# Optimization experiments

Hardware: AMD Instinct MI355X
Metric: run time of the kernel (lower is better)

The kernel has to match this reference:

```python
import jax, jax.numpy as jnp
import numpy as np

WIDTH = 256          # hidden width of FiLM MLP
NUM_FREQ = 8         # NeRF frequencies
BASE_FREQ = 1.25
TWO_PI = 2.0 * np.pi


def _uniform_linear(k, out_dim, in_dim):
    # torch nn.Linear default init: U(-1/sqrt(in), 1/sqrt(in))
    kw, kb = jax.random.split(k)
    s = 1.0 / np.sqrt(in_dim)
    W = jax.random.uniform(kw, (out_dim, in_dim), minval=-s, maxval=s, dtype=jnp.float32)
    b = jax.random.uniform(kb, (out_dim,), minval=-s, maxval=s, dtype=jnp.float32)
    return W, b


def setup_inputs() -> dict:
    key = jax.random.key(0)
    ks = jax.random.split(key, 14)
    B, T = 1024, 512
    latent_dim, lstm_hidden_dim = 128, 128
    spatial_dim, dir_dim, num_directions = 32, 8, 6
    emb_out = 2 * NUM_FREQ + 1                      # 17 (include_input)
    mod_in = latent_dim + lstm_hidden_dim + spatial_dim + dir_dim  # 296
    num_mods = 2 * WIDTH                            # width*(depth-1) = 512

    W_mod, b_mod = _uniform_linear(ks[0], num_mods, mod_in)
    W0, b0 = _uniform_linear(ks[1], WIDTH, emb_out)
    W1, b1 = _uniform_linear(ks[2], WIDTH, WIDTH)
    Wo, bo = _uniform_linear(ks[3], 1, WIDTH)
    Bmat = jax.random.normal(ks[4], (2, 16), dtype=jnp.float32) * 0.1  # sigma=0.1
    Ws1, bs1 = _uniform_linear(ks[5], 64, 32)
    Ws2, bs2 = _uniform_linear(ks[6], spatial_dim, 64)
    dir_emb = jax.random.normal(ks[7], (num_directions, dir_dim), dtype=jnp.float32)

    return dict(
        coords=jax.random.uniform(ks[8], (B, T, 1), dtype=jnp.float32),
        code=jax.random.normal(ks[9], (B, latent_dim), dtype=jnp.float32),
        hs=jax.random.normal(ks[10], (B, T, lstm_hidden_dim), dtype=jnp.float32),
        x_statics=jax.random.normal(ks[11], (B, 2), dtype=jnp.float32),
        dir_idx=jax.random.randint(ks[12], (1024,), 0, num_directions, dtype=jnp.int32),
        W_mod=W_mod, b_mod=b_mod, W0=W0, b0=b0, W1=W1, b1=b1, Wo=Wo, bo=bo,
        Bmat=Bmat, Ws1=Ws1, bs1=bs1, Ws2=Ws2, bs2=bs2, dir_emb=dir_emb,
    )


def reference(coords, code, hs, x_statics, dir_idx,
              W_mod, b_mod, W0, b0, W1, b1, Wo, bo,
              Bmat, Ws1, bs1, Ws2, bs2, dir_emb):
    B, T, _ = coords.shape

    # --- NeRF encoding: (B,T,1) -> (B,T,17) ---
    bands = BASE_FREQ * jnp.arange(0, NUM_FREQ, dtype=coords.dtype)     # (8,)
    winded = (coords[..., None, :] * bands[None, None, :, None]).reshape(B, T, -1)
    pos = jnp.concatenate([coords, jnp.sin(winded), jnp.cos(winded)], axis=-1)

    # --- Static encoder: latlon Fourier MLP + direction embedding ---
    proj = TWO_PI * (x_statics @ Bmat)                                  # (B,16)
    feats = jnp.concatenate([jnp.sin(proj), jnp.cos(proj)], axis=-1)    # (B,32)
    h = jax.nn.gelu(feats @ Ws1.T + bs1, approximate=False)             # (B,64)
    spatial = h @ Ws2.T + bs2                                           # (B,32)
    static_emb = jnp.concatenate([spatial, dir_emb[dir_idx]], axis=-1)  # (B,40)

    # --- Modulations: cat(code, h_t, static) -> 2*WIDTH, vectorized over T ---
    ctx = jnp.concatenate([
        jnp.broadcast_to(code[:, None, :], (B, T, code.shape[-1])),
        hs,
        jnp.broadcast_to(static_emb[:, None, :], (B, T, static_emb.shape[-1])),
    ], axis=-1)                                                         # (B,T,296)
    mods = jnp.einsum('btc,mc->btm', ctx, W_mod) + b_mod                # (B,T,512)

    # --- FiLM(shift)-modulated MLP: relu(Lin(x) + mod_chunk) per hidden layer ---
    x = jax.nn.relu(jnp.einsum('bte,we->btw', pos, W0) + b0 + mods[..., :WIDTH])
    x = jax.nn.relu(jnp.einsum('btw,vw->btv', x, W1) + b1 + mods[..., WIDTH:])
    out = jnp.einsum('btw,ow->bto', x, Wo) + bo                         # (B,T,1)
    return out
```

## Files before the change

kernel.cpp:

```cpp
#include <hip/hip_runtime.h>
#include <math.h>

typedef unsigned short ushort_t;
typedef __bf16 bf16x8 __attribute__((ext_vector_type(8)));
typedef __bf16 bf16x4 __attribute__((ext_vector_type(4)));
typedef float f32x4 __attribute__((ext_vector_type(4)));

#define TWO_PI_F 6.283185307179586f

#define WMT_OFF   0
#define PC_OFF    151552
#define WT0P_OFF  675840
#define WT1P_OFF  696320

__device__ __forceinline__ ushort_t f2bf(float f) {
  unsigned int u = __float_as_uint(f);
  u += 0x7fffu + ((u >> 16) & 1u);
  return (ushort_t)(u >> 16);
}

__global__ void pack_mfma_k(const float* __restrict__ W0,
                            const float* __restrict__ W1,
                            const float* __restrict__ W_mod,
                            float* __restrict__ WmT,
                            ushort_t* __restrict__ WT0p,
                            ushort_t* __restrict__ WT1p) {
  int i0 = blockIdx.x * blockDim.x + threadIdx.x;
  int stride = gridDim.x * blockDim.x;
  for (int idx = i0; idx < 296 * 512; idx += stride) {
    int c = idx >> 9, m = idx & 511;
    WmT[idx] = W_mod[m * 296 + c];
  }
  for (int e = i0; e < 40960; e += stride) {
    int j = e & 7, l = (e >> 3) & 63, nt = (e >> 9) & 15, ks = e >> 13;
    int k = ks * 32 + (l >> 4) * 8 + j;
    int n = nt * 16 + (l & 15);
    float v = 0.0f;
    if (k < 17) v = W0[n * 17 + k];
    else if (k >= 32) v = W_mod[n * 296 + 128 + (k - 32)];
    WT0p[e] = f2bf(v);
  }
  for (int e = i0; e < 98304; e += stride) {
    int j = e & 7, l = (e >> 3) & 63, nt = (e >> 9) & 15, ks = e >> 13;
    int k = ks * 32 + (l >> 4) * 8 + j;
    int n = nt * 16 + (l & 15);
    float v = (k < 256) ? W1[n * 256 + k]
                        : W_mod[(256 + n) * 296 + 128 + (k - 256)];
    WT1p[e] = f2bf(v);
  }
}

__global__ void precompute_pc_k(const float* __restrict__ code,
                                const float* __restrict__ x_statics,
                                const int* __restrict__ dir_idx,
                                const float* __restrict__ WmT,
                                const float* __restrict__ b_mod,
                                const float* __restrict__ b0,
                                const float* __restrict__ b1,
                                const float* __restrict__ Bmat,
                                const float* __restrict__ Ws1,
                                const float* __restrict__ bs1,
                                const float* __restrict__ Ws2,
                                const float* __restrict__ bs2,
                                const float* __restrict__ dir_emb,
                                float* __restrict__ pc) {
  int b = blockIdx.x, t = threadIdx.x;
  __shared__ float feats[32];
  __shared__ float h[64];
  __shared__ float se[40];
  __shared__ float cd[128];
  if (t < 16) {
    float p = TWO_PI_F * (x_statics[2 * b] * Bmat[t] + x_statics[2 * b + 1] * Bmat[16 + t]);
    feats[t] = sinf(p);
    feats[16 + t] = cosf(p);
  }
  if (t >= 128 && t < 256) cd[t - 128] = code[b * 128 + (t - 128)];
  __syncthreads();
  if (t < 64) {
    float a = bs1[t];
#pragma unroll
    for (int c = 0; c < 32; ++c) a = fmaf(feats[c], Ws1[t * 32 + c], a);
    h[t] = 0.5f * a * (1.0f + erff(a * 0.70710678118654752440f));
  }
  __syncthreads();
  if (t < 32) {
    float a = bs2[t];
#pragma unroll
    for (int c = 0; c < 64; ++c) a = fmaf(h[c], Ws2[t * 64 + c], a);
    se[t] = a;
  } else if (t < 40) {
    se[t] = dir_emb[dir_idx[b] * 8 + (t - 32)];
  }
  __syncthreads();
  float a = b_mod[t] + ((t < 256) ? b0[t] : b1[t - 256]);
  for (int c = 0; c < 128; ++c) a = fmaf(cd[c], WmT[c * 512 + t], a);
#pragma unroll
  for (int c = 0; c < 40; ++c) a = fmaf(se[c], WmT[(256 + c) * 512 + t], a);
  pc[b * 512 + t] = a;
}

__global__ __launch_bounds__(512, 6) void film_mfma(
    const float* __restrict__ coords, const float* __restrict__ hs,
    const float* __restrict__ pc, const ushort_t* __restrict__ WT0p,
    const ushort_t* __restrict__ WT1p, const float* __restrict__ Wo,
    const float* __restrict__ bo, float* __restrict__ out) {
  __shared__ uint4 rowbuf4[49152 / 16];
  __shared__ float pcs[512];
  __shared__ float psum[512];
  char* rowbuf = (char*)rowbuf4;

  const int tid = threadIdx.x;
  const int wv = tid >> 6;
  const int l = tid & 63;
  const int l4 = l & 15;
  const int hi4 = l >> 4;
  const size_t row0 = (size_t)blockIdx.x * 64;
  const int b = blockIdx.x >> 3;

  pcs[tid] = pc[(size_t)b * 512 + tid];

  {
    const float4* hsv = (const float4*)(hs + row0 * 128);
#pragma unroll
    for (int it = 0; it < 4; ++it) {
      int idx = it * 512 + tid;
      int r = idx >> 5, c4 = idx & 31;
      float4 v = hsv[idx];
      bf16x4 hb;
      hb[0] = (__bf16)v.x; hb[1] = (__bf16)v.y;
      hb[2] = (__bf16)v.z; hb[3] = (__bf16)v.w;
      int byte = (r * 768 + 512 + c4 * 8) ^ ((r & 7) << 4);
      *(uint2*)(rowbuf + byte) = __builtin_bit_cast(uint2, hb);
    }
  }
  if (tid < 64) {
    int row = tid;
    float c = coords[row0 + row];
    __bf16 pv[32];
    pv[0] = (__bf16)c;
    pv[1] = (__bf16)0.0f;
    pv[9] = (__bf16)1.0f;
#pragma unroll
    for (int f = 1; f < 8; ++f) {
      float s, co;
      __sincosf(1.25f * (float)f * c, &s, &co);
      pv[1 + f] = (__bf16)s;
      pv[9 + f] = (__bf16)co;
    }
#pragma unroll
    for (int k = 17; k < 32; ++k) pv[k] = (__bf16)0.0f;
    int base = row * 768, swz = (row & 7) << 4;
#pragma unroll
    for (int s = 0; s < 4; ++s)
      *(uint4*)(rowbuf + ((base + s * 16) ^ swz)) = *(const uint4*)&pv[s * 8];
  }

  int addrU[4], swzU[4];
#pragma unroll
  for (int mt = 0; mt < 4; ++mt) {
    int row = mt * 16 + l4;
    addrU[mt] = row * 768 + hi4 * 16;
    swzU[mt] = (row & 7) << 4;
  }

  __syncthreads();

  f32x4 acc[4][2];
#pragma unroll
  for (int mt = 0; mt < 4; ++mt)
#pragma unroll
    for (int i = 0; i < 2; ++i) acc[mt][i] = (f32x4){0.f, 0.f, 0.f, 0.f};

  {
    const uint4* Bb = (const uint4*)WT0p;
#pragma unroll
    for (int kk = 0; kk < 5; ++kk) {
      const int ks = (kk < 4) ? (kk + 1) : 0;
      bf16x8 w0 = __builtin_bit_cast(bf16x8, Bb[(ks * 16 + wv * 2 + 0) * 64 + l]);
      bf16x8 w1 = __builtin_bit_cast(bf16x8, Bb[(ks * 16 + wv * 2 + 1) * 64 + l]);
#pragma unroll
      for (int mt = 0; mt < 4; ++mt) {
        bf16x8 u;
        int off = (ks == 0) ? addrU[mt] : (addrU[mt] + 512 + (ks - 1) * 64);
        __builtin_memcpy(&u, rowbuf + (off ^ swzU[mt]), 16);
        acc[mt][0] = __builtin_amdgcn_mfma_f32_16x16x32_bf16(w0, u, acc[mt][0], 0, 0, 0);
        acc[mt][1] = __builtin_amdgcn_mfma_f32_16x16x32_bf16(w1, u, acc[mt][1], 0, 0, 0);
      }
    }
  }
  __syncthreads();

#pragma unroll
  for (int i = 0; i < 2; ++i) {
    int n0 = (wv * 2 + i) * 16 + hi4 * 4;
    float4 p4 = *(const float4*)&pcs[n0];
#pragma unroll
    for (int mt = 0; mt < 4; ++mt) {
      int t = mt * 16 + l4;
      bf16x4 hv;
      hv[0] = (__bf16)fmaxf(acc[mt][i][0] + p4.x, 0.f);
      hv[1] = (__bf16)fmaxf(acc[mt][i][1] + p4.y, 0.f);
      hv[2] = (__bf16)fmaxf(acc[mt][i][2] + p4.z, 0.f);
      hv[3] = (__bf16)fmaxf(acc[mt][i][3] + p4.w, 0.f);
      int byte = (t * 768 + n0 * 2) ^ ((t & 7) << 4);
      *(uint2*)(rowbuf + byte) = __builtin_bit_cast(uint2, hv);
    }
  }
  __syncthreads();

#pragma unroll
  for (int mt = 0; mt < 4; ++mt)
#pragma unroll
    for (int i = 0; i < 2; ++i) acc[mt][i] = (f32x4){0.f, 0.f, 0.f, 0.f};

  {
    const uint4* Bb = (const uint4*)WT1p;
#pragma unroll
    for (int ks = 0; ks < 12; ++ks) {
      bf16x8 w0 = __builtin_bit_cast(bf16x8, Bb[(ks * 16 + wv * 2 + 0) * 64 + l]);
      bf16x8 w1 = __builtin_bit_cast(bf16x8, Bb[(ks * 16 + wv * 2 + 1) * 64 + l]);
#pragma unroll
      for (int mt = 0; mt < 4; ++mt) {
        bf16x8 u;
        __builtin_memcpy(&u, rowbuf + ((addrU[mt] + ks * 64) ^ swzU[mt]), 16);
        acc[mt][0] = __builtin_amdgcn_mfma_f32_16x16x32_bf16(w0, u, acc[mt][0], 0, 0, 0);
        acc[mt][1] = __builtin_amdgcn_mfma_f32_16x16x32_bf16(w1, u, acc[mt][1], 0, 0, 0);
      }
    }
  }

  {
    float4 p4[2], w4[2];
#pragma unroll
    for (int i = 0; i < 2; ++i) {
      int n0 = (wv * 2 + i) * 16 + hi4 * 4;
      p4[i] = *(const float4*)&pcs[256 + n0];
      w4[i] = ((const float4*)Wo)[(wv * 2 + i) * 4 + hi4];
    }
#pragma unroll
    for (int mt = 0; mt < 4; ++mt) {
      float s = 0.f;
#pragma unroll
      for (int i = 0; i < 2; ++i) {
        s += fmaxf(acc[mt][i][0] + p4[i].x, 0.f) * w4[i].x;
        s += fmaxf(acc[mt][i][1] + p4[i].y, 0.f) * w4[i].y;
        s += fmaxf(acc[mt][i][2] + p4[i].z, 0.f) * w4[i].z;
        s += fmaxf(acc[mt][i][3] + p4[i].w, 0.f) * w4[i].w;
      }
      s += __shfl_xor(s, 16);
      s += __shfl_xor(s, 32);
      if (hi4 == 0) psum[wv * 64 + mt * 16 + l4] = s;
    }
  }
  __syncthreads();
  if (tid < 64) {
    float s = bo[0];
#pragma unroll
    for (int w = 0; w < 8; ++w) s += psum[w * 64 + tid];
    out[row0 + tid] = s;
  }
}

extern "C" void kernel_launch(void* const* d_in, const int* in_sizes, int n_in,
                              void* d_out, int out_size, void* d_ws, size_t ws_size,
                              hipStream_t stream) {
  (void)in_sizes; (void)n_in; (void)out_size; (void)ws_size;
  const float* coords    = (const float*)d_in[0];
  const float* code      = (const float*)d_in[1];
  const float* hs        = (const float*)d_in[2];
  const float* x_statics = (const float*)d_in[3];
  const int*   dir_idx   = (const int*)d_in[4];
  const float* W_mod     = (const float*)d_in[5];
  const float* b_mod     = (const float*)d_in[6];
  const float* W0        = (const float*)d_in[7];
  const float* b0        = (const float*)d_in[8];
  const float* W1        = (const float*)d_in[9];
  const float* b1        = (const float*)d_in[10];
  const float* Wo        = (const float*)d_in[11];
  const float* bo        = (const float*)d_in[12];
  const float* Bmat      = (const float*)d_in[13];
  const float* Ws1       = (const float*)d_in[14];
  const float* bs1       = (const float*)d_in[15];
  const float* Ws2       = (const float*)d_in[16];
  const float* bs2       = (const float*)d_in[17];
  const float* dir_emb   = (const float*)d_in[18];
  float* out = (float*)d_out;
  float* wsf = (float*)d_ws;

  float*    WmT  = wsf + WMT_OFF;
  float*    pc   = wsf + PC_OFF;
  ushort_t* WT0p = (ushort_t*)(wsf + WT0P_OFF);
  ushort_t* WT1p = (ushort_t*)(wsf + WT1P_OFF);

  hipLaunchKernelGGL(pack_mfma_k, dim3(1024), dim3(256), 0, stream,
                     W0, W1, W_mod, WmT, WT0p, WT1p);
  hipLaunchKernelGGL(precompute_pc_k, dim3(1024), dim3(512), 0, stream,
                     code, x_statics, dir_idx, WmT, b_mod, b0, b1,
                     Bmat, Ws1, bs1, Ws2, bs2, dir_emb, pc);
  hipLaunchKernelGGL(film_mfma, dim3(8192), dim3(512), 0, stream,
                     coords, hs, pc, WT0p, WT1p, Wo, bo, out);
}
```

Before: 184.2 us.

## Double block tile to 128 rows with 2x4 wave grid and prefetched weight fragments

The main FiLM kernel now processes 128 rows per block instead of 64. Its 8 waves are arranged as 2 row groups by 4 column groups, so each wave holds 4 N-tiles by 4 M-tiles of accumulators. Each weight fragment loaded from global memory is reused across more MFMAs, halving weight traffic per row, and the next k-step's weight fragments are double-buffered in registers. The cost is 96KB of LDS per block and more accumulator registers, which lowers occupancy (launch bounds changed from 6 to 2 blocks per CU).

After: 193.1 us. 1.05x slower.

```diff
diff --git a/kernel.cpp b/kernel.cpp
--- a/kernel.cpp
+++ b/kernel.cpp
@@ -99,12 +99,12 @@
   pc[b * 512 + t] = a;
 }
 
-__global__ __launch_bounds__(512, 6) void film_mfma(
+__global__ __launch_bounds__(512, 2) void film_mfma(
     const float* __restrict__ coords, const float* __restrict__ hs,
     const float* __restrict__ pc, const ushort_t* __restrict__ WT0p,
     const ushort_t* __restrict__ WT1p, const float* __restrict__ Wo,
     const float* __restrict__ bo, float* __restrict__ out) {
-  __shared__ uint4 rowbuf4[49152 / 16];
+  __shared__ uint4 rowbuf4[98304 / 16];
   __shared__ float pcs[512];
   __shared__ float psum[512];
   char* rowbuf = (char*)rowbuf4;
@@ -114,15 +114,17 @@
   const int l = tid & 63;
   const int l4 = l & 15;
   const int hi4 = l >> 4;
-  const size_t row0 = (size_t)blockIdx.x * 64;
-  const int b = blockIdx.x >> 3;
+  const int wr = wv >> 2;
+  const int wc = wv & 3;
+  const size_t row0 = (size_t)blockIdx.x * 128;
+  const int b = blockIdx.x >> 2;
 
   pcs[tid] = pc[(size_t)b * 512 + tid];
 
   {
     const float4* hsv = (const float4*)(hs + row0 * 128);
 #pragma unroll
-    for (int it = 0; it < 4; ++it) {
+    for (int it = 0; it < 8; ++it) {
       int idx = it * 512 + tid;
       int r = idx >> 5, c4 = idx & 31;
       float4 v = hsv[idx];
@@ -133,7 +135,7 @@
       *(uint2*)(rowbuf + byte) = __builtin_bit_cast(uint2, hb);
     }
   }
-  if (tid < 64) {
+  if (tid < 128) {
     int row = tid;
     float c = coords[row0 + row];
     __bf16 pv[32];
@@ -149,54 +151,62 @@
     }
 #pragma unroll
     for (int k = 17; k < 32; ++k) pv[k] = (__bf16)0.0f;
-    int base = row * 768, swz = (row & 7) << 4;
+    int base = row * 768, swzp = (row & 7) << 4;
 #pragma unroll
     for (int s = 0; s < 4; ++s)
-      *(uint4*)(rowbuf + ((base + s * 16) ^ swz)) = *(const uint4*)&pv[s * 8];
-  }
-
-  int addrU[4], swzU[4];
-#pragma unroll
-  for (int mt = 0; mt < 4; ++mt) {
-    int row = mt * 16 + l4;
-    addrU[mt] = row * 768 + hi4 * 16;
-    swzU[mt] = (row & 7) << 4;
-  }
-
-  __syncthreads();
-
-  f32x4 acc[4][2];
+      *(uint4*)(rowbuf + ((base + s * 16) ^ swzp)) = *(const uint4*)&pv[s * 8];
+  }
+
+  const int swz = (l4 & 7) << 4;
+  int addrU[4];
 #pragma unroll
   for (int mt = 0; mt < 4; ++mt)
-#pragma unroll
-    for (int i = 0; i < 2; ++i) acc[mt][i] = (f32x4){0.f, 0.f, 0.f, 0.f};
+    addrU[mt] = (wr * 64 + mt * 16 + l4) * 768 + hi4 * 16;
+
+  __syncthreads();
+
+  f32x4 acc[4][4];
+#pragma unroll
+  for (int mt = 0; mt < 4; ++mt)
+#pragma unroll
+    for (int i = 0; i < 4; ++i) acc[mt][i] = (f32x4){0.f, 0.f, 0.f, 0.f};
 
   {
     const uint4* Bb = (const uint4*)WT0p;
+    bf16x8 wf[2][4];
+#pragma unroll
+    for (int i = 0; i < 4; ++i)
+      wf[0][i] = __builtin_bit_cast(bf16x8, Bb[(1 * 16 + wc * 4 + i) * 64 + l]);
 #pragma unroll
     for (int kk = 0; kk < 5; ++kk) {
       const int ks = (kk < 4) ? (kk + 1) : 0;
-      bf16x8 w0 = __builtin_bit_cast(bf16x8, Bb[(ks * 16 + wv * 2 + 0) * 64 + l]);
-      bf16x8 w1 = __builtin_bit_cast(bf16x8, Bb[(ks * 16 + wv * 2 + 1) * 64 + l]);
+      const int cur = kk & 1;
+      if (kk < 4) {
+        const int ksn = (kk < 3) ? (kk + 2) : 0;
+#pragma unroll
+        for (int i = 0; i < 4; ++i)
+          wf[cur ^ 1][i] = __builtin_bit_cast(bf16x8, Bb[(ksn * 16 + wc * 4 + i) * 64 + l]);
+      }
 #pragma unroll
       for (int mt = 0; mt < 4; ++mt) {
         bf16x8 u;
         int off = (ks == 0) ? addrU[mt] : (addrU[mt] + 512 + (ks - 1) * 64);
-        __builtin_memcpy(&u, rowbuf + (off ^ swzU[mt]), 16);
-        acc[mt][0] = __builtin_amdgcn_mfma_f32_16x16x32_bf16(w0, u, acc[mt][0], 0, 0, 0);
-        acc[mt][1] = __builtin_amdgcn_mfma_f32_16x16x32_bf16(w1, u, acc[mt][1], 0, 0, 0);
-      }
-    }
-  }
-  __syncthreads();
-
-#pragma unroll
-  for (int i = 0; i < 2; ++i) {
-    int n0 = (wv * 2 + i) * 16 + hi4 * 4;
+        __builtin_memcpy(&u, rowbuf + (off ^ swz), 16);
+#pragma unroll
+        for (int i = 0; i < 4; ++i)
+          acc[mt][i] = __builtin_amdgcn_mfma_f32_16x16x32_bf16(wf[cur][i], u, acc[mt][i], 0, 0, 0);
+      }
+    }
+  }
+  __syncthreads();
+
+#pragma unroll
+  for (int i = 0; i < 4; ++i) {
+    int n0 = wc * 64 + i * 16 + hi4 * 4;
     float4 p4 = *(const float4*)&pcs[n0];
 #pragma unroll
     for (int mt = 0; mt < 4; ++mt) {
-      int t = mt * 16 + l4;
+      int t = wr * 64 + mt * 16 + l4;
       bf16x4 hv;
       hv[0] = (__bf16)fmaxf(acc[mt][i][0] + p4.x, 0.f);
       hv[1] = (__bf16)fmaxf(acc[mt][i][1] + p4.y, 0.f);
@@ -211,37 +221,46 @@
 #pragma unroll
   for (int mt = 0; mt < 4; ++mt)
 #pragma unroll
-    for (int i = 0; i < 2; ++i) acc[mt][i] = (f32x4){0.f, 0.f, 0.f, 0.f};
+    for (int i = 0; i < 4; ++i) acc[mt][i] = (f32x4){0.f, 0.f, 0.f, 0.f};
 
   {
     const uint4* Bb = (const uint4*)WT1p;
+    bf16x8 wf[2][4];
+#pragma unroll
+    for (int i = 0; i < 4; ++i)
+      wf[0][i] = __builtin_bit_cast(bf16x8, Bb[(wc * 4 + i) * 64 + l]);
 #pragma unroll
     for (int ks = 0; ks < 12; ++ks) {
-      bf16x8 w0 = __builtin_bit_cast(bf16x8, Bb[(ks * 16 + wv * 2 + 0) * 64 + l]);
-      bf16x8 w1 = __builtin_bit_cast(bf16x8, Bb[(ks * 16 + wv * 2 + 1) * 64 + l]);
+      const int cur = ks & 1;
+      if (ks < 11) {
+#pragma unroll
+        for (int i = 0; i < 4; ++i)
+          wf[cur ^ 1][i] = __builtin_bit_cast(bf16x8, Bb[((ks + 1) * 16 + wc * 4 + i) * 64 + l]);
+      }
 #pragma unroll
       for (int mt = 0; mt < 4; ++mt) {
         bf16x8 u;
-        __builtin_memcpy(&u, rowbuf + ((addrU[mt] + ks * 64) ^ swzU[mt]), 16);
-        acc[mt][0] = __builtin_amdgcn_mfma_f32_16x16x32_bf16(w0, u, acc[mt][0], 0, 0, 0);
-        acc[mt][1] = __builtin_amdgcn_mfma_f32_16x16x32_bf16(w1, u, acc[mt][1], 0, 0, 0);
+        __builtin_memcpy(&u, rowbuf + ((addrU[mt] + ks * 64) ^ swz), 16);
+#pragma unroll
+        for (int i = 0; i < 4; ++i)
+          acc[mt][i] = __builtin_amdgcn_mfma_f32_16x16x32_bf16(wf[cur][i], u, acc[mt][i], 0, 0, 0);
       }
     }
   }
 
   {
-    float4 p4[2], w4[2];
-#pragma unroll
-    for (int i = 0; i < 2; ++i) {
-      int n0 = (wv * 2 + i) * 16 + hi4 * 4;
+    float4 p4[4], w4[4];
+#pragma unroll
+    for (int i = 0; i < 4; ++i) {
+      int n0 = wc * 64 + i * 16 + hi4 * 4;
       p4[i] = *(const float4*)&pcs[256 + n0];
-      w4[i] = ((const float4*)Wo)[(wv * 2 + i) * 4 + hi4];
+      w4[i] = ((const float4*)Wo)[(wc * 4 + i) * 4 + hi4];
     }
 #pragma unroll
     for (int mt = 0; mt < 4; ++mt) {
       float s = 0.f;
 #pragma unroll
-      for (int i = 0; i < 2; ++i) {
+      for (int i = 0; i < 4; ++i) {
         s += fmaxf(acc[mt][i][0] + p4[i].x, 0.f) * w4[i].x;
         s += fmaxf(acc[mt][i][1] + p4[i].y, 0.f) * w4[i].y;
         s += fmaxf(acc[mt][i][2] + p4[i].z, 0.f) * w4[i].z;
@@ -249,14 +268,12 @@
       }
       s += __shfl_xor(s, 16);
       s += __shfl_xor(s, 32);
-      if (hi4 == 0) psum[wv * 64 + mt * 16 + l4] = s;
-    }
-  }
-  __syncthreads();
-  if (tid < 64) {
-    float s = bo[0];
-#pragma unroll
-    for (int w = 0; w < 8; ++w) s += psum[w * 64 + tid];
+      if (hi4 == 0) psum[wc * 128 + wr * 64 + mt * 16 + l4] = s;
+    }
+  }
+  __syncthreads();
+  if (tid < 128) {
+    float s = bo[0] + psum[tid] + psum[128 + tid] + psum[256 + tid] + psum[384 + tid];
     out[row0 + tid] = s;
   }
 }
@@ -297,6 +314,6 @@
   hipLaunchKernelGGL(precompute_pc_k, dim3(1024), dim3(512), 0, stream,
                      code, x_statics, dir_idx, WmT, b_mod, b0, b1,
                      Bmat, Ws1, bs1, Ws2, bs2, dir_emb, pc);
-  hipLaunchKernelGGL(film_mfma, dim3(8192), dim3(512), 0, stream,
+  hipLaunchKernelGGL(film_mfma, dim3(4096), dim3(512), 0, stream,
                      coords, hs, pc, WT0p, WT1p, Wo, bo, out);
 }
```
